# Kernel tuning notes

Measured on AMD Instinct MI355X. Metric: run time of the kernel, lower is better.

Reference implementation:

```python
import jax, jax.numpy as jnp
import numpy as np

NL = 192
SCALE = 1.5
SH_C0 = 0.28209479177387814
SH_C1 = 0.4886025119029199
SH_C2 = [1.0925484305920792, -1.0925484305920792, 0.31539156525252005, -1.0925484305920792, 0.5462742152960396]


def sh_eval(k, d):
    # k: (N, 3, 9) SH coeffs, d: (N, 3) directions -> (N, 3) rgb
    x, y, z = d[..., 0:1], d[..., 1:2], d[..., 2:3]
    return (SH_C0 * k[..., 0]
            - SH_C1 * y * k[..., 1]
            + SH_C1 * z * k[..., 2]
            - SH_C1 * x * k[..., 3]
            + SH_C2[0] * x * y * k[..., 4]
            + SH_C2[1] * y * z * k[..., 5]
            + SH_C2[2] * (2.0 * z * z - x * x - y * y) * k[..., 6]
            + SH_C2[3] * x * z * k[..., 7]
            + SH_C2[4] * (x * x - y * y) * k[..., 8])


def setup_inputs() -> dict:
    key = jax.random.key(0)
    k1, k2 = jax.random.split(key)
    N = 1048576
    x = jax.random.normal(k1, (N, 3), dtype=jnp.float32)
    d = jax.random.normal(k2, (N, 3), dtype=jnp.float32)
    voxel = jnp.ones((NL, NL, NL, 28), dtype=jnp.float32) / 100.0
    return {"x": x, "d": d, "voxel": voxel}


def reference(x, d, voxel):
    xs = x / SCALE
    mask = jnp.all(jnp.abs(xs) < 0.5, axis=1)  # (N,)
    # continuous grid coordinates, clipped like the original
    idx = jnp.clip(xs / (2.0 / NL) + NL / 2.0, 0.0, NL - 1.0)  # (N,3)
    xf = jnp.floor(idx)
    xc = jnp.ceil(idx)
    f = xf.astype(jnp.int32)
    c = xc.astype(jnp.int32)
    # 8 vertices in the ORIGINAL module's ordering (incl. its patch-layout quirk)
    vx = jnp.stack([f[:, 0], c[:, 0], f[:, 0], f[:, 0], f[:, 0], c[:, 0], c[:, 0], c[:, 0]], axis=1)
    vy = jnp.stack([f[:, 1], f[:, 1], c[:, 1], f[:, 1], c[:, 1], f[:, 1], c[:, 1], c[:, 1]], axis=1)
    vz = jnp.stack([f[:, 2], f[:, 2], f[:, 2], c[:, 2], c[:, 2], c[:, 2], f[:, 2], c[:, 2]], axis=1)
    v = voxel[vx, vy, vz]  # (N, 8, 28) gather
    # grid_sample trilinear weights on the 2x2x2 patch: slot j=(dd,hh,ww),
    # w-frac = t0, h-frac = t1, d-frac = t2 (align_corners=False, size 2 => frac = t)
    t = idx - xf  # (N,3)
    t0, t1, t2 = t[:, 0], t[:, 1], t[:, 2]
    u0, u1, u2 = 1.0 - t0, 1.0 - t1, 1.0 - t2
    w = jnp.stack([u2 * u1 * u0, u2 * u1 * t0, u2 * t1 * u0, u2 * t1 * t0,
                   t2 * u1 * u0, t2 * u1 * t0, t2 * t1 * u0, t2 * t1 * t0], axis=1)  # (N,8)
    feat = jnp.einsum('nk,nkc->nc', w, v)  # (N,28)
    sigma = jnp.where(mask, jax.nn.relu(feat[:, 0]), 0.0)  # (N,)
    k = feat[:, 1:].reshape(-1, 3, 9)
    color = jnp.where(mask[:, None], sh_eval(k, d), 0.0)  # (N,3)
    return color, sigma
```

## Files before the change

kernel.cpp:

```cpp
#include <hip/hip_runtime.h>


#define VNL 192
#define BLK 256
#define WPB 4

#define SH_C0f 0.28209479177387814f
#define SH_C1f 0.4886025119029199f
#define C2_0f  1.0925484305920792f
#define C2_1f (-1.0925484305920792f)
#define C2_2f  0.31539156525252005f
#define C2_3f (-1.0925484305920792f)
#define C2_4f  0.5462742152960396f

template <int CTRL>
__device__ __forceinline__ float dpp_add(float v) {
    int s = __builtin_amdgcn_update_dpp(0, __float_as_int(v), CTRL, 0xF, 0xF, true);
    return v + __int_as_float(s);
}

__global__ __launch_bounds__(BLK) void plen_fused_kernel(
    const float* __restrict__ x,
    const float* __restrict__ d,
    const float* __restrict__ voxel,
    float* __restrict__ out,
    int N)
{
    __shared__ __align__(16) float s_pool[BLK][8];
    __shared__ unsigned s_wcnt[WPB];

    const int tid  = threadIdx.x;
    const int i    = blockIdx.x * BLK + tid;
    const int wid  = tid >> 6;
    const int lane = tid & 63;
    const int g = lane >> 3;
    const int j = lane & 7;

    bool act = false;
    float px = 0.f, py = 0.f, pz = 0.f;
    float vdx = 0.f, vdy = 0.f, vdz = 0.f;
    if (i < N) {
        px = x[3 * i + 0] / 1.5f;
        py = x[3 * i + 1] / 1.5f;
        pz = x[3 * i + 2] / 1.5f;
        act = (fabsf(px) < 0.5f) && (fabsf(py) < 0.5f) && (fabsf(pz) < 0.5f);
        vdx = d[3 * i + 0];
        vdy = d[3 * i + 1];
        vdz = d[3 * i + 2];
        if (!act) {
            out[3 * i + 0] = 0.f;
            out[3 * i + 1] = 0.f;
            out[3 * i + 2] = 0.f;
            out[(size_t)3 * N + i] = 0.f;
        }
    }

    unsigned long long bal = __ballot(act);
    unsigned wtot = (unsigned)__popcll(bal);
    unsigned pre  = (unsigned)__popcll(bal & ((1ull << lane) - 1ull));
    if (lane == 0) s_wcnt[wid] = wtot;
    __syncthreads();

    unsigned n0 = s_wcnt[0], n1 = s_wcnt[1], n2 = s_wcnt[2], n3 = s_wcnt[3];
    unsigned M = n0 + n1 + n2 + n3;
    unsigned base = (wid > 0 ? n0 : 0u) + (wid > 1 ? n1 : 0u) + (wid > 2 ? n2 : 0u);

    if (act) {
        unsigned slot = base + pre;
        float4* rp = reinterpret_cast<float4*>(&s_pool[slot][0]);
        rp[0] = make_float4(px, py, pz, __int_as_float(i));
        rp[1] = make_float4(vdx, vdy, vdz, 0.f);
    }
    __syncthreads();

    for (unsigned c = (unsigned)wid; c * 8u < M; c += WPB) {
        unsigned r = c * 8u + (unsigned)g;
        bool gact = (r < M);
        unsigned rr = gact ? r : 0u;

        const float4* rp = reinterpret_cast<const float4*>(&s_pool[rr][0]);
        float4 e0 = rp[0];
        float4 e1 = rp[1];

        if (gact) {
            float ppx = e0.x, ppy = e0.y, ppz = e0.z;
            int   pi  = __float_as_int(e0.w);
            float pdx = e1.x, pdy = e1.y, pdz = e1.z;

            const float step = 2.0f / (float)VNL;
            float ix = fminf(fmaxf(ppx / step + (float)(VNL / 2), 0.0f), (float)(VNL - 1));
            float iy = fminf(fmaxf(ppy / step + (float)(VNL / 2), 0.0f), (float)(VNL - 1));
            float iz = fminf(fmaxf(ppz / step + (float)(VNL / 2), 0.0f), (float)(VNL - 1));

            float fx = floorf(ix), fy = floorf(iy), fz = floorf(iz);
            int f0 = (int)fx, f1 = (int)fy, f2 = (int)fz;
            int c0i = (int)ceilf(ix), c1i = (int)ceilf(iy), c2i = (int)ceilf(iz);

            float t0 = ix - fx, t1 = iy - fy, t2 = iz - fz;
            float u0 = 1.0f - t0, u1 = 1.0f - t1, u2 = 1.0f - t2;

            float wj = ((j & 4) ? t2 : u2) * ((j & 2) ? t1 : u1) * ((j & 1) ? t0 : u0);

            int X = ((0xE2 >> j) & 1) ? c0i : f0;
            int Y = ((0xD4 >> j) & 1) ? c1i : f1;
            int Z = ((0xB8 >> j) & 1) ? c2i : f2;
            int off = ((X * VNL + Y) * VNL + Z) * 112;

            const char* cell = (const char*)voxel + (size_t)(unsigned)off;
            float4 v0 = *(const float4*)(cell +  0);
            float4 v1 = *(const float4*)(cell + 16);
            float4 v2 = *(const float4*)(cell + 32);
            float4 v3 = *(const float4*)(cell + 48);
            float4 v4 = *(const float4*)(cell + 64);
            float4 v5 = *(const float4*)(cell + 80);
            float4 v6 = *(const float4*)(cell + 96);

            float b1 = -SH_C1f * pdy;
            float b2 =  SH_C1f * pdz;
            float b3 = -SH_C1f * pdx;
            float b4 = C2_0f * pdx * pdy;
            float b5 = C2_1f * pdy * pdz;
            float b6 = C2_2f * (2.0f * pdz * pdz - pdx * pdx - pdy * pdy);
            float b7 = C2_3f * pdx * pdz;
            float b8 = C2_4f * (pdx * pdx - pdy * pdy);

            float cc0 = SH_C0f*v0.y + b1*v0.z + b2*v0.w + b3*v1.x + b4*v1.y
                      + b5*v1.z + b6*v1.w + b7*v2.x + b8*v2.y;
            float cc1 = SH_C0f*v2.z + b1*v2.w + b2*v3.x + b3*v3.y + b4*v3.z
                      + b5*v3.w + b6*v4.x + b7*v4.y + b8*v4.z;
            float cc2 = SH_C0f*v4.w + b1*v5.x + b2*v5.y + b3*v5.z + b4*v5.w
                      + b5*v6.x + b6*v6.y + b7*v6.z + b8*v6.w;
            cc0 *= wj; cc1 *= wj; cc2 *= wj;
            float ff0 = wj * v0.x;

            cc0 = dpp_add<0xB1>(cc0); cc1 = dpp_add<0xB1>(cc1);
            cc2 = dpp_add<0xB1>(cc2); ff0 = dpp_add<0xB1>(ff0);
            cc0 = dpp_add<0x4E>(cc0); cc1 = dpp_add<0x4E>(cc1);
            cc2 = dpp_add<0x4E>(cc2); ff0 = dpp_add<0x4E>(ff0);
            cc0 = dpp_add<0x141>(cc0); cc1 = dpp_add<0x141>(cc1);
            cc2 = dpp_add<0x141>(cc2); ff0 = dpp_add<0x141>(ff0);

            if (j < 4) {
                float rv = (j == 0) ? cc0 : (j == 1) ? cc1 : (j == 2) ? cc2
                                                          : fmaxf(ff0, 0.0f);
                size_t a = (j < 3) ? ((size_t)3 * pi + j) : ((size_t)3 * N + pi);
                out[a] = rv;
            }
        }
    }
}

extern "C" void kernel_launch(void* const* d_in, const int* in_sizes, int n_in,
                              void* d_out, int out_size, void* d_ws, size_t ws_size,
                              hipStream_t stream) {
    const float* x     = (const float*)d_in[0];
    const float* d     = (const float*)d_in[1];
    const float* voxel = (const float*)d_in[2];
    float* out = (float*)d_out;
    int N = in_sizes[0] / 3;

    int grid = (N + BLK - 1) / BLK;
    plen_fused_kernel<<<grid, BLK, 0, stream>>>(x, d, voxel, out, N);
}
```

Measured before the change: 47.65 us.

## Compact active points across four tiles per block and dual-issue gathers

Each block now processes four 256-point tiles. Active points from all four are compacted into a larger shared pool, and the grid shrinks by a factor of four. The gather loop handles two 8-point chunks per iteration, issuing both sets of voxel loads before either reduction to add memory-level parallelism. It also precomputes the clipped grid coordinates during compaction. In exchange there are more barriers per block, higher register pressure from two in-flight chunks, and fewer blocks for latency hiding. Inactive lanes clamp to the last valid slot instead of slot 0.

```diff
diff --git a/kernel.cpp b/kernel.cpp
--- a/kernel.cpp
+++ b/kernel.cpp
@@ -4,6 +4,8 @@
 #define VNL 192
 #define BLK 256
 #define WPB 4
+#define TILES 4
+#define PTS (BLK * TILES)
 
 #define SH_C0f 0.28209479177387814f
 #define SH_C1f 0.4886025119029199f
@@ -26,121 +28,181 @@
     float* __restrict__ out,
     int N)
 {
-    __shared__ __align__(16) float s_pool[BLK][8];
+    __shared__ __align__(16) float4 s_pool[PTS][2];
     __shared__ unsigned s_wcnt[WPB];
 
     const int tid  = threadIdx.x;
-    const int i    = blockIdx.x * BLK + tid;
     const int wid  = tid >> 6;
     const int lane = tid & 63;
     const int g = lane >> 3;
     const int j = lane & 7;
-
-    bool act = false;
-    float px = 0.f, py = 0.f, pz = 0.f;
-    float vdx = 0.f, vdy = 0.f, vdz = 0.f;
-    if (i < N) {
-        px = x[3 * i + 0] / 1.5f;
-        py = x[3 * i + 1] / 1.5f;
-        pz = x[3 * i + 2] / 1.5f;
-        act = (fabsf(px) < 0.5f) && (fabsf(py) < 0.5f) && (fabsf(pz) < 0.5f);
-        vdx = d[3 * i + 0];
-        vdy = d[3 * i + 1];
-        vdz = d[3 * i + 2];
-        if (!act) {
-            out[3 * i + 0] = 0.f;
-            out[3 * i + 1] = 0.f;
-            out[3 * i + 2] = 0.f;
-            out[(size_t)3 * N + i] = 0.f;
-        }
+    const int base_i = blockIdx.x * PTS;
+
+    unsigned Mrun = 0;
+    for (int t = 0; t < TILES; ++t) {
+        int i = base_i + t * BLK + tid;
+        bool act = false;
+        float ix = 0.f, iy = 0.f, iz = 0.f;
+        float vdx = 0.f, vdy = 0.f, vdz = 0.f;
+        if (i < N) {
+            float px = x[3 * i + 0] / 1.5f;
+            float py = x[3 * i + 1] / 1.5f;
+            float pz = x[3 * i + 2] / 1.5f;
+            act = (fabsf(px) < 0.5f) && (fabsf(py) < 0.5f) && (fabsf(pz) < 0.5f);
+            vdx = d[3 * i + 0];
+            vdy = d[3 * i + 1];
+            vdz = d[3 * i + 2];
+            if (act) {
+                const float step = 2.0f / (float)VNL;
+                ix = fminf(fmaxf(px / step + (float)(VNL / 2), 0.0f), (float)(VNL - 1));
+                iy = fminf(fmaxf(py / step + (float)(VNL / 2), 0.0f), (float)(VNL - 1));
+                iz = fminf(fmaxf(pz / step + (float)(VNL / 2), 0.0f), (float)(VNL - 1));
+            } else {
+                out[3 * i + 0] = 0.f;
+                out[3 * i + 1] = 0.f;
+                out[3 * i + 2] = 0.f;
+                out[(size_t)3 * N + i] = 0.f;
+            }
+        }
+
+        unsigned long long bal = __ballot(act);
+        unsigned wtot = (unsigned)__popcll(bal);
+        unsigned pre  = (unsigned)__popcll(bal & ((1ull << lane) - 1ull));
+        if (lane == 0) s_wcnt[wid] = wtot;
+        __syncthreads();
+        unsigned n0 = s_wcnt[0], n1 = s_wcnt[1], n2 = s_wcnt[2], n3 = s_wcnt[3];
+        unsigned wbase = Mrun + (wid > 0 ? n0 : 0u) + (wid > 1 ? n1 : 0u)
+                              + (wid > 2 ? n2 : 0u);
+        if (act) {
+            unsigned slot = wbase + pre;
+            s_pool[slot][0] = make_float4(ix, iy, iz, __int_as_float(i));
+            s_pool[slot][1] = make_float4(vdx, vdy, vdz, 0.f);
+        }
+        Mrun += n0 + n1 + n2 + n3;
+        __syncthreads();
     }
 
-    unsigned long long bal = __ballot(act);
-    unsigned wtot = (unsigned)__popcll(bal);
-    unsigned pre  = (unsigned)__popcll(bal & ((1ull << lane) - 1ull));
-    if (lane == 0) s_wcnt[wid] = wtot;
-    __syncthreads();
-
-    unsigned n0 = s_wcnt[0], n1 = s_wcnt[1], n2 = s_wcnt[2], n3 = s_wcnt[3];
-    unsigned M = n0 + n1 + n2 + n3;
-    unsigned base = (wid > 0 ? n0 : 0u) + (wid > 1 ? n1 : 0u) + (wid > 2 ? n2 : 0u);
-
-    if (act) {
-        unsigned slot = base + pre;
-        float4* rp = reinterpret_cast<float4*>(&s_pool[slot][0]);
-        rp[0] = make_float4(px, py, pz, __int_as_float(i));
-        rp[1] = make_float4(vdx, vdy, vdz, 0.f);
-    }
-    __syncthreads();
-
-    for (unsigned c = (unsigned)wid; c * 8u < M; c += WPB) {
-        unsigned r = c * 8u + (unsigned)g;
-        bool gact = (r < M);
-        unsigned rr = gact ? r : 0u;
-
-        const float4* rp = reinterpret_cast<const float4*>(&s_pool[rr][0]);
-        float4 e0 = rp[0];
-        float4 e1 = rp[1];
-
-        if (gact) {
-            float ppx = e0.x, ppy = e0.y, ppz = e0.z;
-            int   pi  = __float_as_int(e0.w);
-            float pdx = e1.x, pdy = e1.y, pdz = e1.z;
-
-            const float step = 2.0f / (float)VNL;
-            float ix = fminf(fmaxf(ppx / step + (float)(VNL / 2), 0.0f), (float)(VNL - 1));
-            float iy = fminf(fmaxf(ppy / step + (float)(VNL / 2), 0.0f), (float)(VNL - 1));
-            float iz = fminf(fmaxf(ppz / step + (float)(VNL / 2), 0.0f), (float)(VNL - 1));
-
-            float fx = floorf(ix), fy = floorf(iy), fz = floorf(iz);
-            int f0 = (int)fx, f1 = (int)fy, f2 = (int)fz;
-            int c0i = (int)ceilf(ix), c1i = (int)ceilf(iy), c2i = (int)ceilf(iz);
-
-            float t0 = ix - fx, t1 = iy - fy, t2 = iz - fz;
-            float u0 = 1.0f - t0, u1 = 1.0f - t1, u2 = 1.0f - t2;
-
-            float wj = ((j & 4) ? t2 : u2) * ((j & 2) ? t1 : u1) * ((j & 1) ? t0 : u0);
-
-            int X = ((0xE2 >> j) & 1) ? c0i : f0;
-            int Y = ((0xD4 >> j) & 1) ? c1i : f1;
-            int Z = ((0xB8 >> j) & 1) ? c2i : f2;
-            int off = ((X * VNL + Y) * VNL + Z) * 112;
-
-            const char* cell = (const char*)voxel + (size_t)(unsigned)off;
-            float4 v0 = *(const float4*)(cell +  0);
-            float4 v1 = *(const float4*)(cell + 16);
-            float4 v2 = *(const float4*)(cell + 32);
-            float4 v3 = *(const float4*)(cell + 48);
-            float4 v4 = *(const float4*)(cell + 64);
-            float4 v5 = *(const float4*)(cell + 80);
-            float4 v6 = *(const float4*)(cell + 96);
-
-            float b1 = -SH_C1f * pdy;
-            float b2 =  SH_C1f * pdz;
-            float b3 = -SH_C1f * pdx;
-            float b4 = C2_0f * pdx * pdy;
-            float b5 = C2_1f * pdy * pdz;
-            float b6 = C2_2f * (2.0f * pdz * pdz - pdx * pdx - pdy * pdy);
-            float b7 = C2_3f * pdx * pdz;
-            float b8 = C2_4f * (pdx * pdx - pdy * pdy);
-
-            float cc0 = SH_C0f*v0.y + b1*v0.z + b2*v0.w + b3*v1.x + b4*v1.y
-                      + b5*v1.z + b6*v1.w + b7*v2.x + b8*v2.y;
-            float cc1 = SH_C0f*v2.z + b1*v2.w + b2*v3.x + b3*v3.y + b4*v3.z
-                      + b5*v3.w + b6*v4.x + b7*v4.y + b8*v4.z;
-            float cc2 = SH_C0f*v4.w + b1*v5.x + b2*v5.y + b3*v5.z + b4*v5.w
-                      + b5*v6.x + b6*v6.y + b7*v6.z + b8*v6.w;
-            cc0 *= wj; cc1 *= wj; cc2 *= wj;
-            float ff0 = wj * v0.x;
-
-            cc0 = dpp_add<0xB1>(cc0); cc1 = dpp_add<0xB1>(cc1);
-            cc2 = dpp_add<0xB1>(cc2); ff0 = dpp_add<0xB1>(ff0);
-            cc0 = dpp_add<0x4E>(cc0); cc1 = dpp_add<0x4E>(cc1);
-            cc2 = dpp_add<0x4E>(cc2); ff0 = dpp_add<0x4E>(ff0);
+    const unsigned M = Mrun;
+    if (M == 0) return;
+    const unsigned nch = (M + 7u) >> 3;
+
+    for (unsigned c = (unsigned)wid; c < nch; c += 2u * WPB) {
+        unsigned cA = c;
+        unsigned cB = c + WPB;
+
+        unsigned rA = cA * 8u + (unsigned)g;
+        bool onA = (rA < M);
+        unsigned rrA = onA ? rA : (M - 1u);
+        float4 a0 = s_pool[rrA][0];
+        float4 a1 = s_pool[rrA][1];
+        float fxA = floorf(a0.x), fyA = floorf(a0.y), fzA = floorf(a0.z);
+        int fA0 = (int)fxA, fA1 = (int)fyA, fA2 = (int)fzA;
+        int cA0 = (int)ceilf(a0.x), cA1 = (int)ceilf(a0.y), cA2 = (int)ceilf(a0.z);
+        float tA0 = a0.x - fxA, tA1 = a0.y - fyA, tA2 = a0.z - fzA;
+        float wjA = ((j & 4) ? tA2 : 1.0f - tA2) * ((j & 2) ? tA1 : 1.0f - tA1)
+                  * ((j & 1) ? tA0 : 1.0f - tA0);
+        int XA = ((0xE2 >> j) & 1) ? cA0 : fA0;
+        int YA = ((0xD4 >> j) & 1) ? cA1 : fA1;
+        int ZA = ((0xB8 >> j) & 1) ? cA2 : fA2;
+        const char* cellA = (const char*)voxel
+            + (size_t)(unsigned)(((XA * VNL + YA) * VNL + ZA) * 112);
+        float4 vA0 = *(const float4*)(cellA +  0);
+        float4 vA1 = *(const float4*)(cellA + 16);
+        float4 vA2 = *(const float4*)(cellA + 32);
+        float4 vA3 = *(const float4*)(cellA + 48);
+        float4 vA4 = *(const float4*)(cellA + 64);
+        float4 vA5 = *(const float4*)(cellA + 80);
+        float4 vA6 = *(const float4*)(cellA + 96);
+
+        unsigned rB = cB * 8u + (unsigned)g;
+        bool onB = (rB < M);
+        unsigned rrB = onB ? rB : (M - 1u);
+        float4 b0 = s_pool[rrB][0];
+        float4 b1 = s_pool[rrB][1];
+        float fxB = floorf(b0.x), fyB = floorf(b0.y), fzB = floorf(b0.z);
+        int fB0 = (int)fxB, fB1 = (int)fyB, fB2 = (int)fzB;
+        int cB0 = (int)ceilf(b0.x), cB1 = (int)ceilf(b0.y), cB2 = (int)ceilf(b0.z);
+        float tB0 = b0.x - fxB, tB1 = b0.y - fyB, tB2 = b0.z - fzB;
+        float wjB = ((j & 4) ? tB2 : 1.0f - tB2) * ((j & 2) ? tB1 : 1.0f - tB1)
+                  * ((j & 1) ? tB0 : 1.0f - tB0);
+        int XB = ((0xE2 >> j) & 1) ? cB0 : fB0;
+        int YB = ((0xD4 >> j) & 1) ? cB1 : fB1;
+        int ZB = ((0xB8 >> j) & 1) ? cB2 : fB2;
+        const char* cellB = (const char*)voxel
+            + (size_t)(unsigned)(((XB * VNL + YB) * VNL + ZB) * 112);
+        float4 vB0 = *(const float4*)(cellB +  0);
+        float4 vB1 = *(const float4*)(cellB + 16);
+        float4 vB2 = *(const float4*)(cellB + 32);
+        float4 vB3 = *(const float4*)(cellB + 48);
+        float4 vB4 = *(const float4*)(cellB + 64);
+        float4 vB5 = *(const float4*)(cellB + 80);
+        float4 vB6 = *(const float4*)(cellB + 96);
+
+        {
+            float pdx = a1.x, pdy = a1.y, pdz = a1.z;
+            float b1c = -SH_C1f * pdy;
+            float b2c =  SH_C1f * pdz;
+            float b3c = -SH_C1f * pdx;
+            float b4c = C2_0f * pdx * pdy;
+            float b5c = C2_1f * pdy * pdz;
+            float b6c = C2_2f * (2.0f * pdz * pdz - pdx * pdx - pdy * pdy);
+            float b7c = C2_3f * pdx * pdz;
+            float b8c = C2_4f * (pdx * pdx - pdy * pdy);
+
+            float cc0 = SH_C0f*vA0.y + b1c*vA0.z + b2c*vA0.w + b3c*vA1.x + b4c*vA1.y
+                      + b5c*vA1.z + b6c*vA1.w + b7c*vA2.x + b8c*vA2.y;
+            float cc1 = SH_C0f*vA2.z + b1c*vA2.w + b2c*vA3.x + b3c*vA3.y + b4c*vA3.z
+                      + b5c*vA3.w + b6c*vA4.x + b7c*vA4.y + b8c*vA4.z;
+            float cc2 = SH_C0f*vA4.w + b1c*vA5.x + b2c*vA5.y + b3c*vA5.z + b4c*vA5.w
+                      + b5c*vA6.x + b6c*vA6.y + b7c*vA6.z + b8c*vA6.w;
+            cc0 *= wjA; cc1 *= wjA; cc2 *= wjA;
+            float ff0 = wjA * vA0.x;
+
+            cc0 = dpp_add<0xB1>(cc0);  cc1 = dpp_add<0xB1>(cc1);
+            cc2 = dpp_add<0xB1>(cc2);  ff0 = dpp_add<0xB1>(ff0);
+            cc0 = dpp_add<0x4E>(cc0);  cc1 = dpp_add<0x4E>(cc1);
+            cc2 = dpp_add<0x4E>(cc2);  ff0 = dpp_add<0x4E>(ff0);
             cc0 = dpp_add<0x141>(cc0); cc1 = dpp_add<0x141>(cc1);
             cc2 = dpp_add<0x141>(cc2); ff0 = dpp_add<0x141>(ff0);
 
-            if (j < 4) {
+            if (onA && j < 4) {
+                int pi = __float_as_int(a0.w);
+                float rv = (j == 0) ? cc0 : (j == 1) ? cc1 : (j == 2) ? cc2
+                                                          : fmaxf(ff0, 0.0f);
+                size_t a = (j < 3) ? ((size_t)3 * pi + j) : ((size_t)3 * N + pi);
+                out[a] = rv;
+            }
+        }
+
+        {
+            float pdx = b1.x, pdy = b1.y, pdz = b1.z;
+            float b1c = -SH_C1f * pdy;
+            float b2c =  SH_C1f * pdz;
+            float b3c = -SH_C1f * pdx;
+            float b4c = C2_0f * pdx * pdy;
+            float b5c = C2_1f * pdy * pdz;
+            float b6c = C2_2f * (2.0f * pdz * pdz - pdx * pdx - pdy * pdy);
+            float b7c = C2_3f * pdx * pdz;
+            float b8c = C2_4f * (pdx * pdx - pdy * pdy);
+
+            float cc0 = SH_C0f*vB0.y + b1c*vB0.z + b2c*vB0.w + b3c*vB1.x + b4c*vB1.y
+                      + b5c*vB1.z + b6c*vB1.w + b7c*vB2.x + b8c*vB2.y;
+            float cc1 = SH_C0f*vB2.z + b1c*vB2.w + b2c*vB3.x + b3c*vB3.y + b4c*vB3.z
+                      + b5c*vB3.w + b6c*vB4.x + b7c*vB4.y + b8c*vB4.z;
+            float cc2 = SH_C0f*vB4.w + b1c*vB5.x + b2c*vB5.y + b3c*vB5.z + b4c*vB5.w
+                      + b5c*vB6.x + b6c*vB6.y + b7c*vB6.z + b8c*vB6.w;
+            cc0 *= wjB; cc1 *= wjB; cc2 *= wjB;
+            float ff0 = wjB * vB0.x;
+
+            cc0 = dpp_add<0xB1>(cc0);  cc1 = dpp_add<0xB1>(cc1);
+            cc2 = dpp_add<0xB1>(cc2);  ff0 = dpp_add<0xB1>(ff0);
+            cc0 = dpp_add<0x4E>(cc0);  cc1 = dpp_add<0x4E>(cc1);
+            cc2 = dpp_add<0x4E>(cc2);  ff0 = dpp_add<0x4E>(ff0);
+            cc0 = dpp_add<0x141>(cc0); cc1 = dpp_add<0x141>(cc1);
+            cc2 = dpp_add<0x141>(cc2); ff0 = dpp_add<0x141>(ff0);
+
+            if (onB && j < 4) {
+                int pi = __float_as_int(b0.w);
                 float rv = (j == 0) ? cc0 : (j == 1) ? cc1 : (j == 2) ? cc2
                                                           : fmaxf(ff0, 0.0f);
                 size_t a = (j < 3) ? ((size_t)3 * pi + j) : ((size_t)3 * N + pi);
@@ -159,6 +221,6 @@
     float* out = (float*)d_out;
     int N = in_sizes[0] / 3;
 
-    int grid = (N + BLK - 1) / BLK;
+    int grid = (N + PTS - 1) / PTS;
     plen_fused_kernel<<<grid, BLK, 0, stream>>>(x, d, voxel, out, N);
 }
```

Measured after the change: 47.77 us. Within noise of the previous version (+0.2%).

## Process four tiles per block with vectorized staging and bulk zero-fill

Applied to the files above, without the earlier changes.

Each block now handles 1024 points in four tiles. x is loaded with coalesced float4 reads into shared memory, and outputs are zero-filled with float4 stores up front, so the old per-inactive-point scalar writes go away. Direction vectors are read only for active points, and grid coordinates are computed before compaction. Active points from all tiles are compacted into one pool, so the 8-lane gather stage has fuller wavefronts. The cost is more shared memory, fewer blocks, and active outputs being written twice (zero, then value).

```diff
diff --git a/kernel.cpp b/kernel.cpp
--- a/kernel.cpp
+++ b/kernel.cpp
@@ -4,6 +4,8 @@
 #define VNL 192
 #define BLK 256
 #define WPB 4
+#define TILES 4
+#define PTS (BLK * TILES)
 
 #define SH_C0f 0.28209479177387814f
 #define SH_C1f 0.4886025119029199f
@@ -26,126 +28,156 @@
     float* __restrict__ out,
     int N)
 {
-    __shared__ __align__(16) float s_pool[BLK][8];
-    __shared__ unsigned s_wcnt[WPB];
+    __shared__ __align__(16) float4 s_pool[PTS][2];
+    __shared__ __align__(16) float  s_xbuf[3 * PTS];
+    __shared__ unsigned s_wcnt[TILES][WPB];
 
     const int tid  = threadIdx.x;
-    const int i    = blockIdx.x * BLK + tid;
     const int wid  = tid >> 6;
     const int lane = tid & 63;
     const int g = lane >> 3;
     const int j = lane & 7;
+    const int base_i = blockIdx.x * PTS;
+    const int rem = N - base_i;
+    const bool full = (rem >= PTS);
 
-    bool act = false;
-    float px = 0.f, py = 0.f, pz = 0.f;
-    float vdx = 0.f, vdy = 0.f, vdz = 0.f;
-    if (i < N) {
-        px = x[3 * i + 0] / 1.5f;
-        py = x[3 * i + 1] / 1.5f;
-        pz = x[3 * i + 2] / 1.5f;
-        act = (fabsf(px) < 0.5f) && (fabsf(py) < 0.5f) && (fabsf(pz) < 0.5f);
-        vdx = d[3 * i + 0];
-        vdy = d[3 * i + 1];
-        vdz = d[3 * i + 2];
-        if (!act) {
-            out[3 * i + 0] = 0.f;
-            out[3 * i + 1] = 0.f;
-            out[3 * i + 2] = 0.f;
-            out[(size_t)3 * N + i] = 0.f;
-        }
+    const float4 z4 = make_float4(0.f, 0.f, 0.f, 0.f);
+
+    if (full && (((3 * base_i) & 3) == 0)) {
+        float4* cf4 = reinterpret_cast<float4*>(out) + ((3 * base_i) >> 2);
+        #pragma unroll
+        for (int k = 0; k < 3; ++k) cf4[k * BLK + tid] = z4;
+    } else {
+        for (int k = tid; k < 3 * (rem < PTS ? rem : PTS); k += BLK)
+            out[3 * base_i + k] = 0.f;
+    }
+    if (full && (((3 * N + base_i) & 3) == 0)) {
+        float4* sf4 = reinterpret_cast<float4*>(out + (size_t)3 * N + base_i);
+        sf4[tid] = z4;
+    } else {
+        for (int k = tid; k < (rem < PTS ? rem : PTS); k += BLK)
+            out[(size_t)3 * N + base_i + k] = 0.f;
     }
 
-    unsigned long long bal = __ballot(act);
-    unsigned wtot = (unsigned)__popcll(bal);
-    unsigned pre  = (unsigned)__popcll(bal & ((1ull << lane) - 1ull));
-    if (lane == 0) s_wcnt[wid] = wtot;
-    __syncthreads();
-
-    unsigned n0 = s_wcnt[0], n1 = s_wcnt[1], n2 = s_wcnt[2], n3 = s_wcnt[3];
-    unsigned M = n0 + n1 + n2 + n3;
-    unsigned base = (wid > 0 ? n0 : 0u) + (wid > 1 ? n1 : 0u) + (wid > 2 ? n2 : 0u);
-
-    if (act) {
-        unsigned slot = base + pre;
-        float4* rp = reinterpret_cast<float4*>(&s_pool[slot][0]);
-        rp[0] = make_float4(px, py, pz, __int_as_float(i));
-        rp[1] = make_float4(vdx, vdy, vdz, 0.f);
+    if (full && (((3 * base_i) & 3) == 0)) {
+        const float4* xf4 = reinterpret_cast<const float4*>(x) + ((3 * base_i) >> 2);
+        float4* sb4 = reinterpret_cast<float4*>(s_xbuf);
+        #pragma unroll
+        for (int k = 0; k < 3; ++k) sb4[k * BLK + tid] = xf4[k * BLK + tid];
+    } else {
+        for (int k = tid; k < 3 * (rem < PTS ? rem : PTS); k += BLK)
+            s_xbuf[k] = x[3 * base_i + k];
     }
     __syncthreads();
 
-    for (unsigned c = (unsigned)wid; c * 8u < M; c += WPB) {
+    unsigned Mrun = 0;
+    for (int t = 0; t < TILES; ++t) {
+        int p = t * BLK + tid;
+        int i = base_i + p;
+        bool act = false;
+        float ix = 0.f, iy = 0.f, iz = 0.f;
+        float vdx = 0.f, vdy = 0.f, vdz = 0.f;
+        if (i < N) {
+            float px = s_xbuf[3 * p + 0] / 1.5f;
+            float py = s_xbuf[3 * p + 1] / 1.5f;
+            float pz = s_xbuf[3 * p + 2] / 1.5f;
+            act = (fabsf(px) < 0.5f) && (fabsf(py) < 0.5f) && (fabsf(pz) < 0.5f);
+            if (act) {
+                const float step = 2.0f / (float)VNL;
+                ix = fminf(fmaxf(px / step + (float)(VNL / 2), 0.0f), (float)(VNL - 1));
+                iy = fminf(fmaxf(py / step + (float)(VNL / 2), 0.0f), (float)(VNL - 1));
+                iz = fminf(fmaxf(pz / step + (float)(VNL / 2), 0.0f), (float)(VNL - 1));
+                vdx = d[3 * i + 0];
+                vdy = d[3 * i + 1];
+                vdz = d[3 * i + 2];
+            }
+        }
+
+        unsigned long long bal = __ballot(act);
+        unsigned wtot = (unsigned)__popcll(bal);
+        unsigned pre  = (unsigned)__popcll(bal & ((1ull << lane) - 1ull));
+        if (lane == 0) s_wcnt[t][wid] = wtot;
+        __syncthreads();
+
+        unsigned n0 = s_wcnt[t][0], n1 = s_wcnt[t][1];
+        unsigned n2 = s_wcnt[t][2], n3 = s_wcnt[t][3];
+        unsigned wbase = Mrun + (wid > 0 ? n0 : 0u) + (wid > 1 ? n1 : 0u)
+                              + (wid > 2 ? n2 : 0u);
+        if (act) {
+            unsigned slot = wbase + pre;
+            s_pool[slot][0] = make_float4(ix, iy, iz, __int_as_float(i));
+            s_pool[slot][1] = make_float4(vdx, vdy, vdz, 0.f);
+        }
+        Mrun += n0 + n1 + n2 + n3;
+    }
+    __syncthreads();
+
+    const unsigned M = Mrun;
+    if (M == 0) return;
+    const unsigned nch = (M + 7u) >> 3;
+
+    for (unsigned c = (unsigned)wid; c < nch; c += WPB) {
         unsigned r = c * 8u + (unsigned)g;
-        bool gact = (r < M);
-        unsigned rr = gact ? r : 0u;
+        bool on = (r < M);
+        unsigned rr = on ? r : (M - 1u);
 
-        const float4* rp = reinterpret_cast<const float4*>(&s_pool[rr][0]);
-        float4 e0 = rp[0];
-        float4 e1 = rp[1];
+        float4 e0 = s_pool[rr][0];
+        float4 e1 = s_pool[rr][1];
 
-        if (gact) {
-            float ppx = e0.x, ppy = e0.y, ppz = e0.z;
-            int   pi  = __float_as_int(e0.w);
-            float pdx = e1.x, pdy = e1.y, pdz = e1.z;
+        float fx = floorf(e0.x), fy = floorf(e0.y), fz = floorf(e0.z);
+        int f0 = (int)fx, f1 = (int)fy, f2 = (int)fz;
+        int c0i = (int)ceilf(e0.x), c1i = (int)ceilf(e0.y), c2i = (int)ceilf(e0.z);
+        float t0 = e0.x - fx, t1 = e0.y - fy, t2 = e0.z - fz;
 
-            const float step = 2.0f / (float)VNL;
-            float ix = fminf(fmaxf(ppx / step + (float)(VNL / 2), 0.0f), (float)(VNL - 1));
-            float iy = fminf(fmaxf(ppy / step + (float)(VNL / 2), 0.0f), (float)(VNL - 1));
-            float iz = fminf(fmaxf(ppz / step + (float)(VNL / 2), 0.0f), (float)(VNL - 1));
+        float wj = ((j & 4) ? t2 : 1.0f - t2) * ((j & 2) ? t1 : 1.0f - t1)
+                 * ((j & 1) ? t0 : 1.0f - t0);
 
-            float fx = floorf(ix), fy = floorf(iy), fz = floorf(iz);
-            int f0 = (int)fx, f1 = (int)fy, f2 = (int)fz;
-            int c0i = (int)ceilf(ix), c1i = (int)ceilf(iy), c2i = (int)ceilf(iz);
+        int X = ((0xE2 >> j) & 1) ? c0i : f0;
+        int Y = ((0xD4 >> j) & 1) ? c1i : f1;
+        int Z = ((0xB8 >> j) & 1) ? c2i : f2;
+        const char* cell = (const char*)voxel
+            + (size_t)(unsigned)(((X * VNL + Y) * VNL + Z) * 112);
 
-            float t0 = ix - fx, t1 = iy - fy, t2 = iz - fz;
-            float u0 = 1.0f - t0, u1 = 1.0f - t1, u2 = 1.0f - t2;
+        float4 v0 = *(const float4*)(cell +  0);
+        float4 v1 = *(const float4*)(cell + 16);
+        float4 v2 = *(const float4*)(cell + 32);
+        float4 v3 = *(const float4*)(cell + 48);
+        float4 v4 = *(const float4*)(cell + 64);
+        float4 v5 = *(const float4*)(cell + 80);
+        float4 v6 = *(const float4*)(cell + 96);
 
-            float wj = ((j & 4) ? t2 : u2) * ((j & 2) ? t1 : u1) * ((j & 1) ? t0 : u0);
+        float pdx = e1.x, pdy = e1.y, pdz = e1.z;
+        float b1c = -SH_C1f * pdy;
+        float b2c =  SH_C1f * pdz;
+        float b3c = -SH_C1f * pdx;
+        float b4c = C2_0f * pdx * pdy;
+        float b5c = C2_1f * pdy * pdz;
+        float b6c = C2_2f * (2.0f * pdz * pdz - pdx * pdx - pdy * pdy);
+        float b7c = C2_3f * pdx * pdz;
+        float b8c = C2_4f * (pdx * pdx - pdy * pdy);
 
-            int X = ((0xE2 >> j) & 1) ? c0i : f0;
-            int Y = ((0xD4 >> j) & 1) ? c1i : f1;
-            int Z = ((0xB8 >> j) & 1) ? c2i : f2;
-            int off = ((X * VNL + Y) * VNL + Z) * 112;
+        float cc0 = SH_C0f*v0.y + b1c*v0.z + b2c*v0.w + b3c*v1.x + b4c*v1.y
+                  + b5c*v1.z + b6c*v1.w + b7c*v2.x + b8c*v2.y;
+        float cc1 = SH_C0f*v2.z + b1c*v2.w + b2c*v3.x + b3c*v3.y + b4c*v3.z
+                  + b5c*v3.w + b6c*v4.x + b7c*v4.y + b8c*v4.z;
+        float cc2 = SH_C0f*v4.w + b1c*v5.x + b2c*v5.y + b3c*v5.z + b4c*v5.w
+                  + b5c*v6.x + b6c*v6.y + b7c*v6.z + b8c*v6.w;
+        cc0 *= wj; cc1 *= wj; cc2 *= wj;
+        float ff0 = wj * v0.x;
 
-            const char* cell = (const char*)voxel + (size_t)(unsigned)off;
-            float4 v0 = *(const float4*)(cell +  0);
-            float4 v1 = *(const float4*)(cell + 16);
-            float4 v2 = *(const float4*)(cell + 32);
-            float4 v3 = *(const float4*)(cell + 48);
-            float4 v4 = *(const float4*)(cell + 64);
-            float4 v5 = *(const float4*)(cell + 80);
-            float4 v6 = *(const float4*)(cell + 96);
+        cc0 = dpp_add<0xB1>(cc0);  cc1 = dpp_add<0xB1>(cc1);
+        cc2 = dpp_add<0xB1>(cc2);  ff0 = dpp_add<0xB1>(ff0);
+        cc0 = dpp_add<0x4E>(cc0);  cc1 = dpp_add<0x4E>(cc1);
+        cc2 = dpp_add<0x4E>(cc2);  ff0 = dpp_add<0x4E>(ff0);
+        cc0 = dpp_add<0x141>(cc0); cc1 = dpp_add<0x141>(cc1);
+        cc2 = dpp_add<0x141>(cc2); ff0 = dpp_add<0x141>(ff0);
 
-            float b1 = -SH_C1f * pdy;
-            float b2 =  SH_C1f * pdz;
-            float b3 = -SH_C1f * pdx;
-            float b4 = C2_0f * pdx * pdy;
-            float b5 = C2_1f * pdy * pdz;
-            float b6 = C2_2f * (2.0f * pdz * pdz - pdx * pdx - pdy * pdy);
-            float b7 = C2_3f * pdx * pdz;
-            float b8 = C2_4f * (pdx * pdx - pdy * pdy);
-
-            float cc0 = SH_C0f*v0.y + b1*v0.z + b2*v0.w + b3*v1.x + b4*v1.y
-                      + b5*v1.z + b6*v1.w + b7*v2.x + b8*v2.y;
-            float cc1 = SH_C0f*v2.z + b1*v2.w + b2*v3.x + b3*v3.y + b4*v3.z
-                      + b5*v3.w + b6*v4.x + b7*v4.y + b8*v4.z;
-            float cc2 = SH_C0f*v4.w + b1*v5.x + b2*v5.y + b3*v5.z + b4*v5.w
-                      + b5*v6.x + b6*v6.y + b7*v6.z + b8*v6.w;
-            cc0 *= wj; cc1 *= wj; cc2 *= wj;
-            float ff0 = wj * v0.x;
-
-            cc0 = dpp_add<0xB1>(cc0); cc1 = dpp_add<0xB1>(cc1);
-            cc2 = dpp_add<0xB1>(cc2); ff0 = dpp_add<0xB1>(ff0);
-            cc0 = dpp_add<0x4E>(cc0); cc1 = dpp_add<0x4E>(cc1);
-            cc2 = dpp_add<0x4E>(cc2); ff0 = dpp_add<0x4E>(ff0);
-            cc0 = dpp_add<0x141>(cc0); cc1 = dpp_add<0x141>(cc1);
-            cc2 = dpp_add<0x141>(cc2); ff0 = dpp_add<0x141>(ff0);
-
-            if (j < 4) {
-                float rv = (j == 0) ? cc0 : (j == 1) ? cc1 : (j == 2) ? cc2
-                                                          : fmaxf(ff0, 0.0f);
-                size_t a = (j < 3) ? ((size_t)3 * pi + j) : ((size_t)3 * N + pi);
-                out[a] = rv;
-            }
+        if (on && j < 4) {
+            int pi = __float_as_int(e0.w);
+            float rv = (j == 0) ? cc0 : (j == 1) ? cc1 : (j == 2) ? cc2
+                                                      : fmaxf(ff0, 0.0f);
+            size_t a = (j < 3) ? ((size_t)3 * pi + j) : ((size_t)3 * N + pi);
+            out[a] = rv;
         }
     }
 }
@@ -159,6 +191,6 @@
     float* out = (float*)d_out;
     int N = in_sizes[0] / 3;
 
-    int grid = (N + BLK - 1) / BLK;
+    int grid = (N + PTS - 1) / PTS;
     plen_fused_kernel<<<grid, BLK, 0, stream>>>(x, d, voxel, out, N);
 }
```

New measurement: 47.89 us. Within noise of the previous version (+0.5%).
